# Optimization experiments

Measured on AMD Instinct MI355X. Metric: run time of the kernel, lower is better.

Reference implementation:

```python
import jax, jax.numpy as jnp
import numpy as np

N = 50000        # nodes
E = 800000       # edges (avg degree 16)
D_IN = 64
D_HID = 128      # 2 * out_dim
D_OUT = 64


def setup_inputs() -> dict:
    key = jax.random.key(0)
    ks = jax.random.split(key, 6)
    x = jax.random.normal(ks[0], (N, D_IN), dtype=jnp.float32)
    edge_index = jax.random.randint(ks[1], (2, E), 0, N, dtype=jnp.int32)
    # Glorot-style init like PyG GCNConv
    W1 = jax.random.normal(ks[2], (D_IN, D_HID), dtype=jnp.float32) / np.sqrt(D_IN)
    b1 = jnp.zeros((D_HID,), dtype=jnp.float32)
    W2 = jax.random.normal(ks[3], (D_HID, D_OUT), dtype=jnp.float32) / np.sqrt(D_HID)
    b2 = jnp.zeros((D_OUT,), dtype=jnp.float32)
    return {"x": x, "edge_index": edge_index, "W1": W1, "b1": b1, "W2": W2, "b2": b2}


def _gcn_norm(edge_index, num_nodes):
    # PyG GCNConv default: add self-loops, symmetric normalization D^-1/2 A_hat D^-1/2
    loop = jnp.arange(num_nodes, dtype=edge_index.dtype)
    src = jnp.concatenate([edge_index[0], loop])
    dst = jnp.concatenate([edge_index[1], loop])
    deg = jax.ops.segment_sum(jnp.ones_like(dst, dtype=jnp.float32), dst,
                              num_segments=num_nodes)
    dinv = jnp.where(deg > 0, jax.lax.rsqrt(deg), 0.0)
    norm = dinv[src] * dinv[dst]  # [E+N]
    return src, dst, norm


def _gcn_conv(x, W, b, src, dst, norm, num_nodes):
    h = x @ W                                      # [N, F_out]
    msg = h[src] * norm[:, None]                   # gather + scale, [E+N, F_out]
    out = jax.ops.segment_sum(msg, dst, num_segments=num_nodes)  # scatter-add
    return out + b


def reference(x, edge_index, W1, b1, W2, b2):
    num_nodes = x.shape[0]
    src, dst, norm = _gcn_norm(edge_index, num_nodes)
    h = _gcn_conv(x, W1, b1, src, dst, norm, num_nodes)
    h = jax.nn.relu(h)
    node_emb = _gcn_conv(h, W2, b2, src, dst, norm, num_nodes)
    return node_emb
```

## Files before the change

### kernel.cpp

```cpp
#include <hip/hip_runtime.h>

typedef unsigned short u16;
typedef unsigned int u32;

typedef __attribute__((ext_vector_type(8))) short bf16x8;
typedef __attribute__((ext_vector_type(4))) float f32x4;

#define BSH 8
#define CAP 5120
#define OVFCAP 8192
#define CHUNK 2048

__device__ __forceinline__ float bf2f(u16 u) {
    return __uint_as_float(((u32)u) << 16);
}
__device__ __forceinline__ u16 f2bf(float f) {
    u32 x = __float_as_uint(f);
    return (u16)((x + 0x7fffu + ((x >> 16) & 1u)) >> 16);
}

__device__ __forceinline__ bool block_isbf(const u16* __restrict__ x, float* sflag) {
    int tid = threadIdx.x;
    if (tid < 64) {
        u16 v = x[tid * 2];
        u32 ex = (v >> 7) & 0xFFu;
        unsigned long long m = __ballot(ex >= 90u && ex <= 140u);
        if (tid == 0) *sflag = (m == ~0ull) ? 1.0f : 0.0f;
    }
    __syncthreads();
    return *sflag != 0.0f;
}

__device__ __forceinline__ void acc8(uint4 w, float* a) {
    a[0] += bf2f((u16)(w.x & 0xFFFFu)); a[1] += bf2f((u16)(w.x >> 16));
    a[2] += bf2f((u16)(w.y & 0xFFFFu)); a[3] += bf2f((u16)(w.y >> 16));
    a[4] += bf2f((u16)(w.z & 0xFFFFu)); a[5] += bf2f((u16)(w.z >> 16));
    a[6] += bf2f((u16)(w.w & 0xFFFFu)); a[7] += bf2f((u16)(w.w >> 16));
}

__device__ __forceinline__ u32 scale2(u32 g, float di) {
    u16 lo = f2bf(bf2f((u16)(g & 0xFFFFu)) * di);
    u16 hi = f2bf(bf2f((u16)(g >> 16)) * di);
    return (u32)lo | ((u32)hi << 16);
}

__global__ __launch_bounds__(256) void k_binA2(
    const int* __restrict__ src, const int* __restrict__ dst,
    int* __restrict__ gcur, u32* __restrict__ staging,
    u32* __restrict__ ovf, int* __restrict__ ovfcur, int E) {
    __shared__ int hcnt[256];
    __shared__ int hbase[256];
    const int tid = threadIdx.x;
    const int e0 = blockIdx.x * CHUNK;
    const int e1 = min(e0 + CHUNK, E);
    hcnt[tid] = 0;
    __syncthreads();
    int dl[8], sl[8];
    const int eb = e0 + tid * 8;
    const bool vec = (eb + 7 < e1) &&
                     ((((size_t)(dst + eb)) | ((size_t)(src + eb))) & 15) == 0;
    if (vec) {
        int4 d0 = ((const int4*)(dst + eb))[0];
        int4 d1 = ((const int4*)(dst + eb))[1];
        int4 s0v = ((const int4*)(src + eb))[0];
        int4 s1v = ((const int4*)(src + eb))[1];
        dl[0] = d0.x; dl[1] = d0.y; dl[2] = d0.z; dl[3] = d0.w;
        dl[4] = d1.x; dl[5] = d1.y; dl[6] = d1.z; dl[7] = d1.w;
        sl[0] = s0v.x; sl[1] = s0v.y; sl[2] = s0v.z; sl[3] = s0v.w;
        sl[4] = s1v.x; sl[5] = s1v.y; sl[6] = s1v.z; sl[7] = s1v.w;
    } else {
#pragma unroll
        for (int k = 0; k < 8; k++) {
            int e = eb + k;
            bool ok = e < e1;
            dl[k] = ok ? dst[e] : -1;
            sl[k] = ok ? src[e] : 0;
        }
    }
#pragma unroll
    for (int k = 0; k < 8; k++)
        if (dl[k] >= 0) atomicAdd(&hcnt[dl[k] >> BSH], 1);
    __syncthreads();
    {
        int c = hcnt[tid];
        hbase[tid] = (c > 0) ? atomicAdd(&gcur[tid], c) : 0;
        hcnt[tid] = 0;
    }
    __syncthreads();
#pragma unroll
    for (int k = 0; k < 8; k++) {
        int d = dl[k];
        if (d < 0) continue;
        int b = d >> BSH;
        int r = atomicAdd(&hcnt[b], 1);
        int p = hbase[b] + r;
        if (p < CAP) {
            staging[(size_t)b * CAP + p] = (u32)sl[k] | ((u32)(d & 255) << 16);
        } else {
            int q = atomicAdd(ovfcur, 1);
            if (q < OVFCAP) ovf[q] = (u32)sl[k] | ((u32)d << 16);
        }
    }
}

__global__ __launch_bounds__(256) void k_bucket(
    const u32* __restrict__ staging, const int* __restrict__ gcur,
    const u32* __restrict__ ovf, const int* __restrict__ ovfcur,
    int* __restrict__ row_start, float* __restrict__ dinv,
    u16* __restrict__ csr, int nbuck,
    const void* __restrict__ W1, const void* __restrict__ b1,
    const void* __restrict__ W2, const void* __restrict__ b2,
    u16* __restrict__ wc,
    const void* __restrict__ x, u16* __restrict__ gxt, int N, int E) {
    __shared__ float sflag;
    __shared__ int hcnt[256];
    __shared__ int hscan[256];
    __shared__ int hcur[256];
    __shared__ int sred[256];
    __shared__ int sbase;
    __shared__ float sdinv[256];
    const int bid = blockIdx.x;
    const int tid = threadIdx.x;
    bool isbf = block_isbf((const u16*)x, &sflag);

    if (bid < nbuck) {
        const int b = bid;
        const int used = min(gcur[b], CAP);
        const u32* st = staging + (size_t)b * CAP;
        const int no = min(ovfcur[0], OVFCAP);
        const int used4 = used >> 2;
        sred[tid] = (tid < b) ? gcur[tid] : 0;
        hcnt[tid] = 0;
        __syncthreads();
        for (int s = 128; s > 0; s >>= 1) {
            if (tid < s) sred[tid] += sred[tid + s];
            __syncthreads();
        }
        if (tid == 0) sbase = sred[0];
        for (int i = tid; i < used4; i += 256) {
            uint4 p4 = ((const uint4*)st)[i];
            atomicAdd(&hcnt[p4.x >> 16], 1);
            atomicAdd(&hcnt[p4.y >> 16], 1);
            atomicAdd(&hcnt[p4.z >> 16], 1);
            atomicAdd(&hcnt[p4.w >> 16], 1);
        }
        for (int i = (used4 << 2) + tid; i < used; i += 256)
            atomicAdd(&hcnt[st[i] >> 16], 1);
        for (int i = tid; i < no; i += 256) {
            u32 pk = ovf[i];
            int d = (int)(pk >> 16);
            if ((d >> BSH) == b) atomicAdd(&hcnt[d & 255], 1);
        }
        __syncthreads();
        int v = hcnt[tid];
        hscan[tid] = v;
        __syncthreads();
        for (int s = 1; s < 256; s <<= 1) {
            int t = (tid >= s) ? hscan[tid - s] : 0;
            __syncthreads();
            hscan[tid] += t;
            __syncthreads();
        }
        int excl = hscan[tid] - v;
        hcur[tid] = excl;
        int base = sbase;
        float dv = rsqrtf((float)(v + 1));
        sdinv[tid] = dv;
        int node = (b << BSH) + tid;
        if (node < N) {
            row_start[node] = base + excl;
            dinv[node] = dv;
        }
        if (b == 0 && tid == 0) row_start[N] = E;
        __syncthreads();
        for (int i = tid; i < used4; i += 256) {
            uint4 p4 = ((const uint4*)st)[i];
            int r0 = atomicAdd(&hcur[p4.x >> 16], 1); csr[base + r0] = (u16)(p4.x & 0xFFFFu);
            int r1 = atomicAdd(&hcur[p4.y >> 16], 1); csr[base + r1] = (u16)(p4.y & 0xFFFFu);
            int r2 = atomicAdd(&hcur[p4.z >> 16], 1); csr[base + r2] = (u16)(p4.z & 0xFFFFu);
            int r3 = atomicAdd(&hcur[p4.w >> 16], 1); csr[base + r3] = (u16)(p4.w & 0xFFFFu);
        }
        for (int i = (used4 << 2) + tid; i < used; i += 256) {
            u32 pk = st[i];
            int r = atomicAdd(&hcur[pk >> 16], 1);
            csr[base + r] = (u16)(pk & 0xFFFFu);
        }
        for (int i = tid; i < no; i += 256) {
            u32 pk = ovf[i];
            int d = (int)(pk >> 16);
            if ((d >> BSH) == b) {
                int r = atomicAdd(&hcur[d & 255], 1);
                csr[base + r] = (u16)(pk & 0xFFFFu);
            }
        }
        const int row0 = b << BSH;
        for (int i = tid; i < 256 * 16; i += 256) {
            int rl = i >> 4;
            int node2 = row0 + rl;
            if (node2 >= N) break;
            int q = i & 15;
            size_t idx = (size_t)node2 * 16 + q;
            float di = sdinv[rl];
            float4 vv;
            if (isbf) {
                ushort4 u = ((const ushort4*)x)[idx];
                vv.x = bf2f(u.x); vv.y = bf2f(u.y); vv.z = bf2f(u.z); vv.w = bf2f(u.w);
            } else {
                vv = ((const float4*)x)[idx];
            }
            ushort4 o;
            o.x = f2bf(vv.x * di); o.y = f2bf(vv.y * di);
            o.z = f2bf(vv.z * di); o.w = f2bf(vv.w * di);
            ((ushort4*)gxt)[idx] = o;
        }
    } else {
        int cb = bid - nbuck;
        for (int i = cb * 256 + tid; i < 16576; i += 17 * 256) {
            const void* s; int off;
            if (i < 8192)       { int nn = i >> 6, k = i & 63;  s = W1; off = k * 128 + nn; }
            else if (i < 16384) { int j = i - 8192; int nn = j >> 7, k = j & 127; s = W2; off = k * 64 + nn; }
            else if (i < 16512) { s = b1; off = i - 16384; }
            else                { s = b2; off = i - 16512; }
            wc[i] = isbf ? ((const u16*)s)[off] : f2bf(((const float*)s)[off]);
        }
    }
}

template<bool FINAL>
__global__ __launch_bounds__(256) void k_gather(
    const uint4* __restrict__ feat, const int* __restrict__ row_start,
    const u16* __restrict__ csr, const float* __restrict__ dinv,
    const u16* __restrict__ b2c, const void* __restrict__ xdet,
    void* __restrict__ outp, int n) {
    __shared__ float sflag;
    bool isbf = true;
    if (FINAL) isbf = block_isbf((const u16*)xdet, &sflag);
    int t = blockIdx.x * 256 + threadIdx.x;
    int d = t >> 3;
    int lane = t & 7;
    if (d >= n) return;
    const uint4* fl = feat + lane;
    float a[8];
    {
        uint4 w = fl[(size_t)d * 8];
        a[0] = bf2f((u16)(w.x & 0xFFFFu)); a[1] = bf2f((u16)(w.x >> 16));
        a[2] = bf2f((u16)(w.y & 0xFFFFu)); a[3] = bf2f((u16)(w.y >> 16));
        a[4] = bf2f((u16)(w.z & 0xFFFFu)); a[5] = bf2f((u16)(w.z >> 16));
        a[6] = bf2f((u16)(w.w & 0xFFFFu)); a[7] = bf2f((u16)(w.w >> 16));
    }
    int s0 = row_start[d], s1 = row_start[d + 1];
    int j = s0;
    int cur = (j + lane < s1) ? (int)csr[j + lane] : 0;
    while (j + 8 <= s1) {
        int nxt = (j + 8 + lane < s1) ? (int)csr[j + 8 + lane] : 0;
        uint4 wv[8];
#pragma unroll
        for (int u = 0; u < 8; u++) {
            int sv = __shfl(cur, u, 8);
            wv[u] = fl[(size_t)sv * 8];
        }
#pragma unroll
        for (int u = 0; u < 8; u++) acc8(wv[u], a);
        cur = nxt;
        j += 8;
    }
    int rem = s1 - j;
    if (rem > 0) {
        for (int u = 0; u < rem; u++) {
            int sv = __shfl(cur, u, 8);
            uint4 wv = fl[(size_t)sv * 8];
            acc8(wv, a);
        }
    }
    if (FINAL) {
        float di = dinv[d];
#pragma unroll
        for (int u = 0; u < 8; u++)
            a[u] = a[u] * di + bf2f(b2c[8 * lane + u]);
        if (isbf) {
            uint4 o;
            o.x = (u32)f2bf(a[0]) | ((u32)f2bf(a[1]) << 16);
            o.y = (u32)f2bf(a[2]) | ((u32)f2bf(a[3]) << 16);
            o.z = (u32)f2bf(a[4]) | ((u32)f2bf(a[5]) << 16);
            o.w = (u32)f2bf(a[6]) | ((u32)f2bf(a[7]) << 16);
            ((uint4*)outp)[(size_t)d * 8 + lane] = o;
        } else {
            float4* op = (float4*)outp;
            op[(size_t)d * 16 + 2 * lane]     = make_float4(a[0], a[1], a[2], a[3]);
            op[(size_t)d * 16 + 2 * lane + 1] = make_float4(a[4], a[5], a[6], a[7]);
        }
    } else {
        uint4 o;
        o.x = (u32)f2bf(a[0]) | ((u32)f2bf(a[1]) << 16);
        o.y = (u32)f2bf(a[2]) | ((u32)f2bf(a[3]) << 16);
        o.z = (u32)f2bf(a[4]) | ((u32)f2bf(a[5]) << 16);
        o.w = (u32)f2bf(a[6]) | ((u32)f2bf(a[7]) << 16);
        ((uint4*)outp)[(size_t)d * 8 + lane] = o;
    }
}

__global__ __launch_bounds__(256) void k_mlp(
    const u16* __restrict__ accin, const u16* __restrict__ wc,
    const float* __restrict__ dinv, u16* outb, int n) {
    __shared__ __align__(16) u16 As[64 * 72];
    __shared__ __align__(16) u16 W1t[128 * 72];
    __shared__ __align__(16) u16 W2t[64 * 136];
    __shared__ __align__(16) u16 Hs[64 * 136];
    __shared__ float b1s[128];
    __shared__ float dvs[64];
    const int tid = threadIdx.x;
    const int row0 = blockIdx.x * 64;

    if (tid < 64) {
        int r = row0 + tid;
        dvs[tid] = (r < n) ? dinv[r] : 0.f;
    } else if (tid < 192) {
        b1s[tid - 64] = bf2f(wc[16384 + tid - 64]);
    }
    for (int i = tid; i < 512; i += 256) {
        int r = i >> 3, kk = i & 7;
        int row = row0 + r;
        uint4 v = make_uint4(0, 0, 0, 0);
        if (row < n) {
            uint4 g = ((const uint4*)accin)[(size_t)row * 8 + kk];
            float di = dinv[row];
            v.x = scale2(g.x, di); v.y = scale2(g.y, di);
            v.z = scale2(g.z, di); v.w = scale2(g.w, di);
        }
        *(uint4*)&As[r * 72 + kk * 8] = v;
    }
    for (int i = tid; i < 1024; i += 256) {
        int nn = i >> 3, kk = i & 7;
        *(uint4*)&W1t[nn * 72 + kk * 8] = ((const uint4*)wc)[i];
    }
    for (int i = tid; i < 1024; i += 256) {
        int nn = i >> 4, kk = i & 15;
        *(uint4*)&W2t[nn * 136 + kk * 8] = ((const uint4*)(wc + 8192))[i];
    }
    __syncthreads();

    const int wave = tid >> 6;
    const int lane = tid & 63;
    const int q = lane >> 4;
    const int ln = lane & 15;

    bf16x8 a[4][2];
#pragma unroll
    for (int mt = 0; mt < 4; mt++)
#pragma unroll
        for (int ks = 0; ks < 2; ks++)
            a[mt][ks] = *(const bf16x8*)&As[(mt * 16 + ln) * 72 + ks * 32 + q * 8];

    f32x4 c1[2][4];
#pragma unroll
    for (int ntl = 0; ntl < 2; ntl++)
#pragma unroll
        for (int mt = 0; mt < 4; mt++) c1[ntl][mt] = (f32x4){0.f, 0.f, 0.f, 0.f};

#pragma unroll
    for (int ntl = 0; ntl < 2; ntl++) {
        int nt = wave * 2 + ntl;
        bf16x8 b0 = *(const bf16x8*)&W1t[(nt * 16 + ln) * 72 + 0 + q * 8];
        bf16x8 b1f = *(const bf16x8*)&W1t[(nt * 16 + ln) * 72 + 32 + q * 8];
#pragma unroll
        for (int mt = 0; mt < 4; mt++) {
            c1[ntl][mt] = __builtin_amdgcn_mfma_f32_16x16x32_bf16(a[mt][0], b0, c1[ntl][mt], 0, 0, 0);
            c1[ntl][mt] = __builtin_amdgcn_mfma_f32_16x16x32_bf16(a[mt][1], b1f, c1[ntl][mt], 0, 0, 0);
        }
    }
#pragma unroll
    for (int ntl = 0; ntl < 2; ntl++) {
        int col = (wave * 2 + ntl) * 16 + ln;
        float bb = b1s[col];
#pragma unroll
        for (int mt = 0; mt < 4; mt++)
#pragma unroll
            for (int r = 0; r < 4; r++) {
                int hrow = mt * 16 + q * 4 + r;
                Hs[hrow * 136 + col] = f2bf(fmaxf(c1[ntl][mt][r] + bb, 0.f));
            }
    }
    __syncthreads();

    f32x4 c2[4];
#pragma unroll
    for (int mt = 0; mt < 4; mt++) c2[mt] = (f32x4){0.f, 0.f, 0.f, 0.f};
#pragma unroll
    for (int ks = 0; ks < 4; ks++) {
        bf16x8 bb = *(const bf16x8*)&W2t[(wave * 16 + ln) * 136 + ks * 32 + q * 8];
#pragma unroll
        for (int mt = 0; mt < 4; mt++) {
            bf16x8 aa = *(const bf16x8*)&Hs[(mt * 16 + ln) * 136 + ks * 32 + q * 8];
            c2[mt] = __builtin_amdgcn_mfma_f32_16x16x32_bf16(aa, bb, c2[mt], 0, 0, 0);
        }
    }
#pragma unroll
    for (int mt = 0; mt < 4; mt++)
#pragma unroll
        for (int r = 0; r < 4; r++) {
            int rloc = mt * 16 + q * 4 + r;
            int row = row0 + rloc;
            if (row < n) {
                int col = wave * 16 + ln;
                outb[(size_t)row * 64 + col] = f2bf(c2[mt][r] * dvs[rloc]);
            }
        }
}

extern "C" void kernel_launch(void* const* d_in, const int* in_sizes, int n_in,
                              void* d_out, int out_size, void* d_ws, size_t ws_size,
                              hipStream_t stream) {
    const void* x  = d_in[0];
    const int* ei  = (const int*)d_in[1];
    const void* W1 = d_in[2];
    const void* b1 = d_in[3];
    const void* W2 = d_in[4];
    const void* b2 = d_in[5];

    const int N = in_sizes[0] / 64;
    const int E = in_sizes[1] / 2;
    const int* src = ei;
    const int* dst = ei + E;

    float* ws = (float*)d_ws;
    const int NP = ((N + 64) + 63) & ~63;
    float* dinv    = ws;
    int* gcur      = (int*)(ws + NP);
    int* ovfcur    = gcur + 256;
    int* row_start = gcur + 320;
    u32* ovf       = (u32*)(row_start + ((N + 64) & ~63));
    u16* csr       = (u16*)(ovf + OVFCAP);
    u16* wc        = (u16*)(((size_t)(csr + E) + 255) & ~(size_t)255);
    u16* bufB      = (u16*)(((size_t)(wc + 16576) + 255) & ~(size_t)255);
    u32* staging   = (u32*)bufB;
    u16* gxt       = (u16*)d_out;

    const int gth = (N * 8 + 255) / 256;
    const int nbuck = (N + 255) >> BSH;
    const int binB = (E + CHUNK - 1) / CHUNK;
    dim3 blk(256);

    hipMemsetAsync(gcur, 0, 320 * sizeof(int), stream);
    k_binA2<<<dim3(binB), blk, 0, stream>>>(src, dst, gcur, staging, ovf, ovfcur, E);
    k_bucket<<<dim3(nbuck + 17), blk, 0, stream>>>(staging, gcur, ovf, ovfcur,
                                                   row_start, dinv, csr, nbuck,
                                                   W1, b1, W2, b2, wc, x, gxt, N, E);
    k_gather<false><<<dim3(gth), blk, 0, stream>>>((const uint4*)gxt, row_start, csr,
                                                   dinv, wc + 16512, x, bufB, N);
    k_mlp<<<dim3((N + 63) / 64), blk, 0, stream>>>((const u16*)bufB, wc, dinv, bufB, N);
    k_gather<true><<<dim3(gth), blk, 0, stream>>>((const uint4*)bufB, row_start, csr,
                                                  dinv, wc + 16512, x, d_out, N);
}
```

Before: 147.8 us.

## Stage CSR segment in LDS, fold dinv into aggregation, shrink MLP LDS

The bucket kernel now scatters CSR column indices into an LDS staging array and writes them to global memory in one coalesced pass, falling back to direct global stores past SEGCAP. The non-final aggregation multiplies by dinv before storing, so the MLP kernel no longer rescales its input. The MLP kernel aliases the W2 tile onto the As buffer, holding W2 in registers until after the first GEMM, and adds a launch-bounds occupancy hint. It also raises wave priority around the MFMA loops. Together these aim to cut scattered global writes and LDS footprint, at the cost of an extra barrier and more registers.

```diff
diff --git a/kernel.cpp b/kernel.cpp
--- a/kernel.cpp
+++ b/kernel.cpp
@@ -10,6 +10,7 @@
 #define CAP 5120
 #define OVFCAP 8192
 #define CHUNK 2048
+#define SEGCAP 6144
 
 __device__ __forceinline__ float bf2f(u16 u) {
     return __uint_as_float(((u32)u) << 16);
@@ -36,12 +37,6 @@
     a[2] += bf2f((u16)(w.y & 0xFFFFu)); a[3] += bf2f((u16)(w.y >> 16));
     a[4] += bf2f((u16)(w.z & 0xFFFFu)); a[5] += bf2f((u16)(w.z >> 16));
     a[6] += bf2f((u16)(w.w & 0xFFFFu)); a[7] += bf2f((u16)(w.w >> 16));
-}
-
-__device__ __forceinline__ u32 scale2(u32 g, float di) {
-    u16 lo = f2bf(bf2f((u16)(g & 0xFFFFu)) * di);
-    u16 hi = f2bf(bf2f((u16)(g >> 16)) * di);
-    return (u32)lo | ((u32)hi << 16);
 }
 
 __global__ __launch_bounds__(256) void k_binA2(
@@ -119,6 +114,7 @@
     __shared__ int sred[256];
     __shared__ int sbase;
     __shared__ float sdinv[256];
+    __shared__ u16 seg_lds[SEGCAP];
     const int bid = blockIdx.x;
     const int tid = threadIdx.x;
     bool isbf = block_isbf((const u16*)x, &sflag);
@@ -175,23 +171,38 @@
         __syncthreads();
         for (int i = tid; i < used4; i += 256) {
             uint4 p4 = ((const uint4*)st)[i];
-            int r0 = atomicAdd(&hcur[p4.x >> 16], 1); csr[base + r0] = (u16)(p4.x & 0xFFFFu);
-            int r1 = atomicAdd(&hcur[p4.y >> 16], 1); csr[base + r1] = (u16)(p4.y & 0xFFFFu);
-            int r2 = atomicAdd(&hcur[p4.z >> 16], 1); csr[base + r2] = (u16)(p4.z & 0xFFFFu);
-            int r3 = atomicAdd(&hcur[p4.w >> 16], 1); csr[base + r3] = (u16)(p4.w & 0xFFFFu);
+            int r0 = atomicAdd(&hcur[p4.x >> 16], 1);
+            u16 v0 = (u16)(p4.x & 0xFFFFu);
+            if (r0 < SEGCAP) seg_lds[r0] = v0; else csr[base + r0] = v0;
+            int r1 = atomicAdd(&hcur[p4.y >> 16], 1);
+            u16 v1 = (u16)(p4.y & 0xFFFFu);
+            if (r1 < SEGCAP) seg_lds[r1] = v1; else csr[base + r1] = v1;
+            int r2 = atomicAdd(&hcur[p4.z >> 16], 1);
+            u16 v2 = (u16)(p4.z & 0xFFFFu);
+            if (r2 < SEGCAP) seg_lds[r2] = v2; else csr[base + r2] = v2;
+            int r3 = atomicAdd(&hcur[p4.w >> 16], 1);
+            u16 v3 = (u16)(p4.w & 0xFFFFu);
+            if (r3 < SEGCAP) seg_lds[r3] = v3; else csr[base + r3] = v3;
         }
         for (int i = (used4 << 2) + tid; i < used; i += 256) {
             u32 pk = st[i];
             int r = atomicAdd(&hcur[pk >> 16], 1);
-            csr[base + r] = (u16)(pk & 0xFFFFu);
+            u16 vv = (u16)(pk & 0xFFFFu);
+            if (r < SEGCAP) seg_lds[r] = vv; else csr[base + r] = vv;
         }
         for (int i = tid; i < no; i += 256) {
             u32 pk = ovf[i];
             int d = (int)(pk >> 16);
             if ((d >> BSH) == b) {
                 int r = atomicAdd(&hcur[d & 255], 1);
-                csr[base + r] = (u16)(pk & 0xFFFFu);
+                u16 vv = (u16)(pk & 0xFFFFu);
+                if (r < SEGCAP) seg_lds[r] = vv; else csr[base + r] = vv;
             }
+        }
+        __syncthreads();
+        {
+            int seg = min(hscan[255], SEGCAP);
+            for (int i = tid; i < seg; i += 256) csr[base + i] = seg_lds[i];
         }
         const int row0 = b << BSH;
         for (int i = tid; i < 256 * 16; i += 256) {
@@ -272,8 +283,8 @@
             acc8(wv, a);
         }
     }
+    float di = dinv[d];
     if (FINAL) {
-        float di = dinv[d];
 #pragma unroll
         for (int u = 0; u < 8; u++)
             a[u] = a[u] * di + bf2f(b2c[8 * lane + u]);
@@ -291,52 +302,48 @@
         }
     } else {
         uint4 o;
-        o.x = (u32)f2bf(a[0]) | ((u32)f2bf(a[1]) << 16);
-        o.y = (u32)f2bf(a[2]) | ((u32)f2bf(a[3]) << 16);
-        o.z = (u32)f2bf(a[4]) | ((u32)f2bf(a[5]) << 16);
-        o.w = (u32)f2bf(a[6]) | ((u32)f2bf(a[7]) << 16);
+        o.x = (u32)f2bf(a[0] * di) | ((u32)f2bf(a[1] * di) << 16);
+        o.y = (u32)f2bf(a[2] * di) | ((u32)f2bf(a[3] * di) << 16);
+        o.z = (u32)f2bf(a[4] * di) | ((u32)f2bf(a[5] * di) << 16);
+        o.w = (u32)f2bf(a[6] * di) | ((u32)f2bf(a[7] * di) << 16);
         ((uint4*)outp)[(size_t)d * 8 + lane] = o;
     }
 }
 
-__global__ __launch_bounds__(256) void k_mlp(
+__global__ __launch_bounds__(256, 3) void k_mlp(
     const u16* __restrict__ accin, const u16* __restrict__ wc,
     const float* __restrict__ dinv, u16* outb, int n) {
-    __shared__ __align__(16) u16 As[64 * 72];
-    __shared__ __align__(16) u16 W1t[128 * 72];
-    __shared__ __align__(16) u16 W2t[64 * 136];
+    __shared__ __align__(16) u16 U[64 * 72 + 128 * 72];
     __shared__ __align__(16) u16 Hs[64 * 136];
     __shared__ float b1s[128];
     __shared__ float dvs[64];
+    u16* As  = U;
+    u16* W1t = U + 64 * 72;
+    u16* W2t = U;
+
     const int tid = threadIdx.x;
     const int row0 = blockIdx.x * 64;
 
+    for (int i = tid; i < 1024; i += 256) {
+        int nn = i >> 3, kk = i & 7;
+        *(uint4*)&W1t[nn * 72 + kk * 8] = ((const uint4*)wc)[i];
+    }
+    if (tid < 128) b1s[tid] = bf2f(wc[16384 + tid]);
     if (tid < 64) {
         int r = row0 + tid;
         dvs[tid] = (r < n) ? dinv[r] : 0.f;
-    } else if (tid < 192) {
-        b1s[tid - 64] = bf2f(wc[16384 + tid - 64]);
     }
     for (int i = tid; i < 512; i += 256) {
         int r = i >> 3, kk = i & 7;
         int row = row0 + r;
         uint4 v = make_uint4(0, 0, 0, 0);
-        if (row < n) {
-            uint4 g = ((const uint4*)accin)[(size_t)row * 8 + kk];
-            float di = dinv[row];
-            v.x = scale2(g.x, di); v.y = scale2(g.y, di);
-            v.z = scale2(g.z, di); v.w = scale2(g.w, di);
-        }
+        if (row < n) v = ((const uint4*)accin)[(size_t)row * 8 + kk];
         *(uint4*)&As[r * 72 + kk * 8] = v;
     }
-    for (int i = tid; i < 1024; i += 256) {
-        int nn = i >> 3, kk = i & 7;
-        *(uint4*)&W1t[nn * 72 + kk * 8] = ((const uint4*)wc)[i];
-    }
-    for (int i = tid; i < 1024; i += 256) {
-        int nn = i >> 4, kk = i & 15;
-        *(uint4*)&W2t[nn * 136 + kk * 8] = ((const uint4*)(wc + 8192))[i];
-    }
+    uint4 wreg[4];
+#pragma unroll
+    for (int u = 0; u < 4; u++) wreg[u] = ((const uint4*)(wc + 8192))[tid + 256 * u];
+
     __syncthreads();
 
     const int wave = tid >> 6;
@@ -357,6 +364,7 @@
 #pragma unroll
         for (int mt = 0; mt < 4; mt++) c1[ntl][mt] = (f32x4){0.f, 0.f, 0.f, 0.f};
 
+    __builtin_amdgcn_s_setprio(1);
 #pragma unroll
     for (int ntl = 0; ntl < 2; ntl++) {
         int nt = wave * 2 + ntl;
@@ -368,6 +376,7 @@
             c1[ntl][mt] = __builtin_amdgcn_mfma_f32_16x16x32_bf16(a[mt][1], b1f, c1[ntl][mt], 0, 0, 0);
         }
     }
+    __builtin_amdgcn_s_setprio(0);
 #pragma unroll
     for (int ntl = 0; ntl < 2; ntl++) {
         int col = (wave * 2 + ntl) * 16 + ln;
@@ -382,9 +391,18 @@
     }
     __syncthreads();
 
+#pragma unroll
+    for (int u = 0; u < 4; u++) {
+        int i = tid + 256 * u;
+        int nn = i >> 4, kk = i & 15;
+        *(uint4*)&W2t[nn * 136 + kk * 8] = wreg[u];
+    }
+    __syncthreads();
+
     f32x4 c2[4];
 #pragma unroll
     for (int mt = 0; mt < 4; mt++) c2[mt] = (f32x4){0.f, 0.f, 0.f, 0.f};
+    __builtin_amdgcn_s_setprio(1);
 #pragma unroll
     for (int ks = 0; ks < 4; ks++) {
         bf16x8 bb = *(const bf16x8*)&W2t[(wave * 16 + ln) * 136 + ks * 32 + q * 8];
@@ -394,6 +412,7 @@
             c2[mt] = __builtin_amdgcn_mfma_f32_16x16x32_bf16(aa, bb, c2[mt], 0, 0, 0);
         }
     }
+    __builtin_amdgcn_s_setprio(0);
 #pragma unroll
     for (int mt = 0; mt < 4; mt++)
 #pragma unroll
```

Result: slower. 151.8 us (+2.7%).
